# Optimization experiments

Hardware: AMD Instinct MI355X
Metric: run time of the kernel (lower is better)

Reference implementation:

```python
import jax, jax.numpy as jnp
import numpy as np

NEG_BIG = -9e15
ALPHA = 0.2  # LeakyReLU negative slope


def setup_inputs() -> dict:
    key = jax.random.key(0)
    k1, k2, k3, k4 = jax.random.split(key, 4)
    B, N, Fin, Fout = 4, 2048, 128, 128
    h = jax.random.normal(k1, (B, N, Fin), dtype=jnp.float32)
    adj = jax.random.randint(k2, (N, N), 0, 2, dtype=jnp.int32)
    W = jax.random.normal(k3, (Fin, Fout), dtype=jnp.float32) * 0.1
    a = jax.random.normal(k4, (2 * Fout, 1), dtype=jnp.float32) * 0.1
    return {"h": h, "adj": adj, "W": W, "a": a}


def reference(h, adj, W, a):
    # Wh: [B, N, Fout]
    Wh = jnp.einsum('bnf,fo->bno', h, W)
    Fout = W.shape[1]
    a1 = a[:Fout, 0]   # attends to source i
    a2 = a[Fout:, 0]   # attends to target j
    # Decomposed form of leakyrelu(cat([Wh_i, Wh_j]) @ a):
    # e_ij = leakyrelu(a1.Wh_i + a2.Wh_j)  -> [B, N, N]
    f1 = Wh @ a1  # [B, N]
    f2 = Wh @ a2  # [B, N]
    e = jax.nn.leaky_relu(f1[:, :, None] + f2[:, None, :], negative_slope=ALPHA)
    attention = jnp.where(adj[None, :, :] > 0, e, jnp.float32(NEG_BIG))
    attention = jax.nn.softmax(attention, axis=2)
    # dropout is identity in eval mode
    h_prime = jnp.einsum('bij,bjo->bio', attention, Wh)
    return h_prime
```

## Files before the change

kernel.cpp:

```cpp
#include <hip/hip_runtime.h>

#define BB 4
#define NN 2048
#define FF 128
#define NP 2176
#define ALPHA 0.2f
#define SHIFT_C 16.0f

typedef short bf16x8 __attribute__((ext_vector_type(8)));
typedef float f32x4 __attribute__((ext_vector_type(4)));
typedef unsigned u32;

__device__ inline short f2bf(float f) {
    union { float f; unsigned u; } v; v.f = f;
    unsigned r = (v.u + 0x7FFFu + ((v.u >> 16) & 1u)) >> 16;
    return (short)r;
}
__device__ inline float bf2f(short s) {
    union { float f; unsigned u; } v;
    v.u = ((unsigned)(unsigned short)s) << 16;
    return v.f;
}

__global__ __launch_bounds__(256) void k_wh(const float* __restrict__ h,
                                            const float* __restrict__ W,
                                            const float* __restrict__ a,
                                            const int* __restrict__ adj,
                                            short* __restrict__ WhHiT,
                                            short* __restrict__ WhLoT,
                                            float* __restrict__ f1,
                                            float* __restrict__ f2,
                                            u32* __restrict__ adjp) {
    __shared__ float Wa[2 * FF];
    __shared__ float hs[16 * 132];
    int tid = threadIdx.x;
    int r0 = blockIdx.x * 16;

    {
        int fin = tid & 127;
        const float* av = (tid < 128) ? a : (a + FF);
        const float* wr = W + (size_t)fin * FF;
        float s = 0.f;
        for (int o = 0; o < FF; o += 4) {
            float4 wv = *(const float4*)(wr + o);
            float4 avv = *(const float4*)(av + o);
            s += wv.x * avv.x + wv.y * avv.y + wv.z * avv.z + wv.w * avv.w;
        }
        Wa[(tid < 128 ? 0 : FF) + fin] = s;
    }
    {
        const float4* src = (const float4*)(h + (size_t)r0 * FF);
        float4* dst = (float4*)hs;
        dst[tid] = src[tid];
        dst[256 + tid] = src[256 + tid];
    }
    {
        int g = blockIdx.x * 256 + tid;
        int row = g >> 6, wd = g & 63;
        const int4* ar = (const int4*)(adj + (size_t)row * NN + wd * 32);
        u32 word = 0;
#pragma unroll
        for (int q = 0; q < 8; ++q) {
            int4 v = ar[q];
            word |= (u32)(v.x > 0) << (q * 4);
            word |= (u32)(v.y > 0) << (q * 4 + 1);
            word |= (u32)(v.z > 0) << (q * 4 + 2);
            word |= (u32)(v.w > 0) << (q * 4 + 3);
        }
        adjp[row * 64 + wd] = word;
    }
    __syncthreads();

    {
        int w = tid >> 6, lane = tid & 63;
        float wa1_0 = Wa[lane], wa1_1 = Wa[lane + 64];
        float wa2_0 = Wa[FF + lane], wa2_1 = Wa[FF + lane + 64];
        for (int rr = 0; rr < 4; ++rr) {
            int rloc = w * 4 + rr;
            int row = r0 + rloc;
            float x0 = hs[rloc * FF + lane], x1 = hs[rloc * FF + lane + 64];
            float s1 = x0 * wa1_0 + x1 * wa1_1;
            float s2 = x0 * wa2_0 + x1 * wa2_1;
#pragma unroll
            for (int m = 32; m >= 1; m >>= 1) {
                s1 += __shfl_xor(s1, m, 64);
                s2 += __shfl_xor(s2, m, 64);
            }
            if (lane == 0) { f1[row] = s1; f2[row] = s2; }
        }
    }

    int f4 = (tid & 31) * 4;
    int rg = tid >> 5;
    float acc[2][4];
#pragma unroll
    for (int rr = 0; rr < 2; ++rr)
#pragma unroll
        for (int cc = 0; cc < 4; ++cc) acc[rr][cc] = 0.f;

    for (int k0 = 0; k0 < FF; k0 += 4) {
        float4 wv[4];
#pragma unroll
        for (int kk = 0; kk < 4; ++kk)
            wv[kk] = *(const float4*)(W + (size_t)(k0 + kk) * FF + f4);
        float4 hv[2];
#pragma unroll
        for (int rr = 0; rr < 2; ++rr)
            hv[rr] = *(const float4*)(hs + (rg * 2 + rr) * FF + k0);
#pragma unroll
        for (int rr = 0; rr < 2; ++rr) {
            float hk[4] = {hv[rr].x, hv[rr].y, hv[rr].z, hv[rr].w};
#pragma unroll
            for (int kk = 0; kk < 4; ++kk) {
                acc[rr][0] += hk[kk] * wv[kk].x;
                acc[rr][1] += hk[kk] * wv[kk].y;
                acc[rr][2] += hk[kk] * wv[kk].z;
                acc[rr][3] += hk[kk] * wv[kk].w;
            }
        }
    }

    __syncthreads();
    {
#pragma unroll
        for (int rr = 0; rr < 2; ++rr)
            *(float4*)(hs + (rg * 2 + rr) * 132 + f4) =
                make_float4(acc[rr][0], acc[rr][1], acc[rr][2], acc[rr][3]);
    }
    __syncthreads();
    {
        int fo = tid >> 1, jh = tid & 1;
        bf16x8 hv_, lv_;
#pragma unroll
        for (int jj = 0; jj < 8; ++jj) {
            float v = hs[(jh * 8 + jj) * 132 + fo];
            short hh = f2bf(v);
            hv_[jj] = hh;
            lv_[jj] = f2bf(v - bf2f(hh));
        }
        int b = r0 >> 11;
        int j0 = (r0 & (NN - 1)) + jh * 8;
        size_t off = (size_t)(b * FF + fo) * NP + j0;
        *(bf16x8*)(WhHiT + off) = hv_;
        *(bf16x8*)(WhLoT + off) = lv_;
    }
}

#define EV(f2v, f1v, wv, bi) ({ float _t = (f1v) + (f2v); float _x = fmaxf(_t, ALPHA * _t); \
    __expf(_x - SHIFT_C) * (float)(((wv) >> (bi)) & 1u); })

__global__ __launch_bounds__(512, 4) void k_attn(const short* __restrict__ WhHiT,
                                                 const short* __restrict__ WhLoT,
                                                 const u32* __restrict__ adjp,
                                                 const float* __restrict__ f1,
                                                 const float* __restrict__ f2,
                                                 float* __restrict__ out) {
    __shared__ __align__(16) char lds[66688];
    float* row_ps = (float*)(lds + 65536);
    float* row_inv = (float*)(lds + 66560);

    int tid = threadIdx.x;
    int w = tid >> 6, lane = tid & 63;
    int blk = blockIdx.x;
    int b = blk >> 7;
    int tile = (blk >> 1) & 63;
    int half = blk & 1;
    int i0 = tile * 32;

    int r_c = lane & 15, kg = lane >> 4;

    const float* f2b = f2 + b * NN;
    float f10 = f1[b * NN + i0 + r_c];
    float f11 = f1[b * NN + i0 + 16 + r_c];
    const u32* ap0 = adjp + (size_t)(i0 + r_c) * 64;
    const u32* ap1 = adjp + (size_t)(i0 + 16 + r_c) * 64;

    const ptrdiff_t dLo = (ptrdiff_t)BB * FF * NP;
    int s0 = w * 8;
    const short* pB0 = WhHiT + (size_t)(b * FF + half * 64 + 0 * 16 + r_c) * NP + s0 * 32 + kg * 8;
    const short* pB1 = WhHiT + (size_t)(b * FF + half * 64 + 1 * 16 + r_c) * NP + s0 * 32 + kg * 8;
    const short* pB2 = WhHiT + (size_t)(b * FF + half * 64 + 2 * 16 + r_c) * NP + s0 * 32 + kg * 8;
    const short* pB3 = WhHiT + (size_t)(b * FF + half * 64 + 3 * 16 + r_c) * NP + s0 * 32 + kg * 8;

    f32x4 acc0_0 = {0,0,0,0}, acc0_1 = {0,0,0,0};
    f32x4 acc1_0 = {0,0,0,0}, acc1_1 = {0,0,0,0};
    f32x4 acc2_0 = {0,0,0,0}, acc2_1 = {0,0,0,0};
    f32x4 acc3_0 = {0,0,0,0}, acc3_1 = {0,0,0,0};
    float sp0 = 0.f, sp1 = 0.f;

    float4 q0 = *(const float4*)(f2b + s0 * 32 + kg * 8);
    float4 q1 = *(const float4*)(f2b + s0 * 32 + kg * 8 + 4);
    u32 w0 = ap0[s0], w1 = ap1[s0];

#pragma unroll
    for (int s8 = 0; s8 < 8; ++s8) {
        bf16x8 bh0 = *(const bf16x8*)(pB0); bf16x8 bl0 = *(const bf16x8*)(pB0 + dLo);
        bf16x8 bh1 = *(const bf16x8*)(pB1); bf16x8 bl1 = *(const bf16x8*)(pB1 + dLo);
        bf16x8 bh2 = *(const bf16x8*)(pB2); bf16x8 bl2 = *(const bf16x8*)(pB2 + dLo);
        bf16x8 bh3 = *(const bf16x8*)(pB3); bf16x8 bl3 = *(const bf16x8*)(pB3 + dLo);
        int sn = (s0 + s8 + 1) & 63;
        float4 nq0 = *(const float4*)(f2b + sn * 32 + kg * 8);
        float4 nq1 = *(const float4*)(f2b + sn * 32 + kg * 8 + 4);
        u32 nw0 = ap0[sn], nw1 = ap1[sn];

        union { u32 u[4]; bf16x8 v; } A0, A1;
        int bb = kg * 8;
        {
            float pa, pb;
            pa = EV(q0.x, f10, w0, bb + 0); pb = EV(q0.y, f10, w0, bb + 1);
            sp0 += pa + pb;
            asm("v_cvt_pk_bf16_f32 %0, %1, %2" : "=v"(A0.u[0]) : "v"(pa), "v"(pb));
            pa = EV(q0.z, f10, w0, bb + 2); pb = EV(q0.w, f10, w0, bb + 3);
            sp0 += pa + pb;
            asm("v_cvt_pk_bf16_f32 %0, %1, %2" : "=v"(A0.u[1]) : "v"(pa), "v"(pb));
            pa = EV(q1.x, f10, w0, bb + 4); pb = EV(q1.y, f10, w0, bb + 5);
            sp0 += pa + pb;
            asm("v_cvt_pk_bf16_f32 %0, %1, %2" : "=v"(A0.u[2]) : "v"(pa), "v"(pb));
            pa = EV(q1.z, f10, w0, bb + 6); pb = EV(q1.w, f10, w0, bb + 7);
            sp0 += pa + pb;
            asm("v_cvt_pk_bf16_f32 %0, %1, %2" : "=v"(A0.u[3]) : "v"(pa), "v"(pb));

            pa = EV(q0.x, f11, w1, bb + 0); pb = EV(q0.y, f11, w1, bb + 1);
            sp1 += pa + pb;
            asm("v_cvt_pk_bf16_f32 %0, %1, %2" : "=v"(A1.u[0]) : "v"(pa), "v"(pb));
            pa = EV(q0.z, f11, w1, bb + 2); pb = EV(q0.w, f11, w1, bb + 3);
            sp1 += pa + pb;
            asm("v_cvt_pk_bf16_f32 %0, %1, %2" : "=v"(A1.u[1]) : "v"(pa), "v"(pb));
            pa = EV(q1.x, f11, w1, bb + 4); pb = EV(q1.y, f11, w1, bb + 5);
            sp1 += pa + pb;
            asm("v_cvt_pk_bf16_f32 %0, %1, %2" : "=v"(A1.u[2]) : "v"(pa), "v"(pb));
            pa = EV(q1.z, f11, w1, bb + 6); pb = EV(q1.w, f11, w1, bb + 7);
            sp1 += pa + pb;
            asm("v_cvt_pk_bf16_f32 %0, %1, %2" : "=v"(A1.u[3]) : "v"(pa), "v"(pb));
        }

        acc0_0 = __builtin_amdgcn_mfma_f32_16x16x32_bf16(A0.v, bh0, acc0_0, 0, 0, 0);
        acc0_0 = __builtin_amdgcn_mfma_f32_16x16x32_bf16(A0.v, bl0, acc0_0, 0, 0, 0);
        acc0_1 = __builtin_amdgcn_mfma_f32_16x16x32_bf16(A1.v, bh0, acc0_1, 0, 0, 0);
        acc0_1 = __builtin_amdgcn_mfma_f32_16x16x32_bf16(A1.v, bl0, acc0_1, 0, 0, 0);
        acc1_0 = __builtin_amdgcn_mfma_f32_16x16x32_bf16(A0.v, bh1, acc1_0, 0, 0, 0);
        acc1_0 = __builtin_amdgcn_mfma_f32_16x16x32_bf16(A0.v, bl1, acc1_0, 0, 0, 0);
        acc1_1 = __builtin_amdgcn_mfma_f32_16x16x32_bf16(A1.v, bh1, acc1_1, 0, 0, 0);
        acc1_1 = __builtin_amdgcn_mfma_f32_16x16x32_bf16(A1.v, bl1, acc1_1, 0, 0, 0);
        acc2_0 = __builtin_amdgcn_mfma_f32_16x16x32_bf16(A0.v, bh2, acc2_0, 0, 0, 0);
        acc2_0 = __builtin_amdgcn_mfma_f32_16x16x32_bf16(A0.v, bl2, acc2_0, 0, 0, 0);
        acc2_1 = __builtin_amdgcn_mfma_f32_16x16x32_bf16(A1.v, bh2, acc2_1, 0, 0, 0);
        acc2_1 = __builtin_amdgcn_mfma_f32_16x16x32_bf16(A1.v, bl2, acc2_1, 0, 0, 0);
        acc3_0 = __builtin_amdgcn_mfma_f32_16x16x32_bf16(A0.v, bh3, acc3_0, 0, 0, 0);
        acc3_0 = __builtin_amdgcn_mfma_f32_16x16x32_bf16(A0.v, bl3, acc3_0, 0, 0, 0);
        acc3_1 = __builtin_amdgcn_mfma_f32_16x16x32_bf16(A1.v, bh3, acc3_1, 0, 0, 0);
        acc3_1 = __builtin_amdgcn_mfma_f32_16x16x32_bf16(A1.v, bl3, acc3_1, 0, 0, 0);

        pB0 += 32; pB1 += 32; pB2 += 32; pB3 += 32;
        q0 = nq0; q1 = nq1; w0 = nw0; w1 = nw1;
    }

    sp0 += __shfl_xor(sp0, 16, 64); sp0 += __shfl_xor(sp0, 32, 64);
    sp1 += __shfl_xor(sp1, 16, 64); sp1 += __shfl_xor(sp1, 32, 64);
    if (lane < 16) {
        row_ps[w * 32 + lane] = sp0;
        row_ps[w * 32 + 16 + lane] = sp1;
    }
    {
        char* img = lds + w * 8192;
#define STACC(NI, MI, A) { int ch = (((NI)*16 + r_c) * 8 + (MI)*4 + kg) ^ (r_c & 7); \
                           *(f32x4*)(img + ch * 16) = (A); }
        STACC(0, 0, acc0_0) STACC(0, 1, acc0_1)
        STACC(1, 0, acc1_0) STACC(1, 1, acc1_1)
        STACC(2, 0, acc2_0) STACC(2, 1, acc2_1)
        STACC(3, 0, acc3_0) STACC(3, 1, acc3_1)
#undef STACC
    }
    __syncthreads();
    if (tid < 32) {
        float t = 0.f;
#pragma unroll
        for (int ww = 0; ww < 8; ++ww) t += row_ps[ww * 32 + tid];
        row_inv[tid] = 1.0f / t;
    }
    __syncthreads();

    {
        int colg = w * 8 + (lane >> 3);
        int rq = lane & 7;
        int ch = (colg * 8 + rq) ^ (colg & 7);
        f32x4 v = {0, 0, 0, 0};
#pragma unroll
        for (int im = 0; im < 8; ++im)
            v += *(const f32x4*)(lds + im * 8192 + ch * 16);
        f32x4 rinv = *(const f32x4*)((char*)row_inv + rq * 16);
        float* ob = out + ((size_t)b * NN + i0 + rq * 4) * FF + half * 64 + colg;
#pragma unroll
        for (int q = 0; q < 4; ++q)
            ob[(size_t)q * FF] = v[q] * rinv[q];
    }
}

extern "C" void kernel_launch(void* const* d_in, const int* in_sizes, int n_in,
                              void* d_out, int out_size, void* d_ws, size_t ws_size,
                              hipStream_t stream) {
    const float* h   = (const float*)d_in[0];
    const int*   adj = (const int*)d_in[1];
    const float* W   = (const float*)d_in[2];
    const float* a   = (const float*)d_in[3];
    float* out = (float*)d_out;

    short* WhHiT = (short*)d_ws;
    short* WhLoT = WhHiT + (size_t)BB * FF * NP;
    float* f1 = (float*)(WhLoT + (size_t)BB * FF * NP);
    float* f2 = f1 + (size_t)BB * NN;
    u32* adjp = (u32*)(f2 + (size_t)BB * NN);

    k_wh<<<(BB * NN) / 16, 256, 0, stream>>>(h, W, a, adj, WhHiT, WhLoT, f1, f2, adjp);
    k_attn<<<512, 512, 0, stream>>>(WhHiT, WhLoT, adjp, f1, f2, out);
}
```

Measured before the change: 129.3 us.

## Retile attention blocks to 64 rows by 32 output columns

Each block now covers 64 query rows and a quarter of the output features (32 columns) instead of 32 rows and half the features. Each wave builds four attention A-fragments and loads two Wh B-fragment pairs instead of two A-fragments and four B pairs. This cuts global loads of the transposed Wh per block and increases exp/softmax work per block. In exchange the exponentials for each row are recomputed across four column-quarter blocks instead of two, roughly doubling the total VALU exp work. The LDS reduction layout and row-sum buffers are resized to match.

After: 124.4 us (median of 2 runs). -3.8%, faster.

```diff
diff --git a/kernel.cpp b/kernel.cpp
--- a/kernel.cpp
+++ b/kernel.cpp
@@ -149,147 +149,138 @@
 #define EV(f2v, f1v, wv, bi) ({ float _t = (f1v) + (f2v); float _x = fmaxf(_t, ALPHA * _t); \
     __expf(_x - SHIFT_C) * (float)(((wv) >> (bi)) & 1u); })
 
+#define BUILD_A(Adst, F1V, WV, SP) { \
+    float pa, pb; \
+    pa = EV(q0.x, F1V, WV, bb + 0); pb = EV(q0.y, F1V, WV, bb + 1); \
+    SP += pa + pb; \
+    asm("v_cvt_pk_bf16_f32 %0, %1, %2" : "=v"(Adst.u[0]) : "v"(pa), "v"(pb)); \
+    pa = EV(q0.z, F1V, WV, bb + 2); pb = EV(q0.w, F1V, WV, bb + 3); \
+    SP += pa + pb; \
+    asm("v_cvt_pk_bf16_f32 %0, %1, %2" : "=v"(Adst.u[1]) : "v"(pa), "v"(pb)); \
+    pa = EV(q1.x, F1V, WV, bb + 4); pb = EV(q1.y, F1V, WV, bb + 5); \
+    SP += pa + pb; \
+    asm("v_cvt_pk_bf16_f32 %0, %1, %2" : "=v"(Adst.u[2]) : "v"(pa), "v"(pb)); \
+    pa = EV(q1.z, F1V, WV, bb + 6); pb = EV(q1.w, F1V, WV, bb + 7); \
+    SP += pa + pb; \
+    asm("v_cvt_pk_bf16_f32 %0, %1, %2" : "=v"(Adst.u[3]) : "v"(pa), "v"(pb)); }
+
 __global__ __launch_bounds__(512, 4) void k_attn(const short* __restrict__ WhHiT,
                                                  const short* __restrict__ WhLoT,
                                                  const u32* __restrict__ adjp,
                                                  const float* __restrict__ f1,
                                                  const float* __restrict__ f2,
                                                  float* __restrict__ out) {
-    __shared__ __align__(16) char lds[66688];
+    __shared__ __align__(16) char lds[67840];
     float* row_ps = (float*)(lds + 65536);
-    float* row_inv = (float*)(lds + 66560);
+    float* row_inv = (float*)(lds + 67584);
 
     int tid = threadIdx.x;
     int w = tid >> 6, lane = tid & 63;
     int blk = blockIdx.x;
     int b = blk >> 7;
-    int tile = (blk >> 1) & 63;
-    int half = blk & 1;
-    int i0 = tile * 32;
+    int tile = (blk >> 2) & 31;
+    int qt = blk & 3;
+    int i0 = tile * 64;
 
     int r_c = lane & 15, kg = lane >> 4;
 
     const float* f2b = f2 + b * NN;
     float f10 = f1[b * NN + i0 + r_c];
     float f11 = f1[b * NN + i0 + 16 + r_c];
+    float f12 = f1[b * NN + i0 + 32 + r_c];
+    float f13 = f1[b * NN + i0 + 48 + r_c];
     const u32* ap0 = adjp + (size_t)(i0 + r_c) * 64;
     const u32* ap1 = adjp + (size_t)(i0 + 16 + r_c) * 64;
+    const u32* ap2 = adjp + (size_t)(i0 + 32 + r_c) * 64;
+    const u32* ap3 = adjp + (size_t)(i0 + 48 + r_c) * 64;
 
     const ptrdiff_t dLo = (ptrdiff_t)BB * FF * NP;
     int s0 = w * 8;
-    const short* pB0 = WhHiT + (size_t)(b * FF + half * 64 + 0 * 16 + r_c) * NP + s0 * 32 + kg * 8;
-    const short* pB1 = WhHiT + (size_t)(b * FF + half * 64 + 1 * 16 + r_c) * NP + s0 * 32 + kg * 8;
-    const short* pB2 = WhHiT + (size_t)(b * FF + half * 64 + 2 * 16 + r_c) * NP + s0 * 32 + kg * 8;
-    const short* pB3 = WhHiT + (size_t)(b * FF + half * 64 + 3 * 16 + r_c) * NP + s0 * 32 + kg * 8;
-
-    f32x4 acc0_0 = {0,0,0,0}, acc0_1 = {0,0,0,0};
-    f32x4 acc1_0 = {0,0,0,0}, acc1_1 = {0,0,0,0};
-    f32x4 acc2_0 = {0,0,0,0}, acc2_1 = {0,0,0,0};
-    f32x4 acc3_0 = {0,0,0,0}, acc3_1 = {0,0,0,0};
-    float sp0 = 0.f, sp1 = 0.f;
+    const short* pB0 = WhHiT + (size_t)(b * FF + qt * 32 + 0 * 16 + r_c) * NP + s0 * 32 + kg * 8;
+    const short* pB1 = WhHiT + (size_t)(b * FF + qt * 32 + 1 * 16 + r_c) * NP + s0 * 32 + kg * 8;
+
+    f32x4 acc0_0 = {0,0,0,0}, acc0_1 = {0,0,0,0}, acc0_2 = {0,0,0,0}, acc0_3 = {0,0,0,0};
+    f32x4 acc1_0 = {0,0,0,0}, acc1_1 = {0,0,0,0}, acc1_2 = {0,0,0,0}, acc1_3 = {0,0,0,0};
+    float sp0 = 0.f, sp1 = 0.f, sp2 = 0.f, sp3 = 0.f;
 
     float4 q0 = *(const float4*)(f2b + s0 * 32 + kg * 8);
     float4 q1 = *(const float4*)(f2b + s0 * 32 + kg * 8 + 4);
-    u32 w0 = ap0[s0], w1 = ap1[s0];
+    u32 w0 = ap0[s0], w1 = ap1[s0], w2 = ap2[s0], w3 = ap3[s0];
 
 #pragma unroll
     for (int s8 = 0; s8 < 8; ++s8) {
         bf16x8 bh0 = *(const bf16x8*)(pB0); bf16x8 bl0 = *(const bf16x8*)(pB0 + dLo);
         bf16x8 bh1 = *(const bf16x8*)(pB1); bf16x8 bl1 = *(const bf16x8*)(pB1 + dLo);
-        bf16x8 bh2 = *(const bf16x8*)(pB2); bf16x8 bl2 = *(const bf16x8*)(pB2 + dLo);
-        bf16x8 bh3 = *(const bf16x8*)(pB3); bf16x8 bl3 = *(const bf16x8*)(pB3 + dLo);
         int sn = (s0 + s8 + 1) & 63;
         float4 nq0 = *(const float4*)(f2b + sn * 32 + kg * 8);
         float4 nq1 = *(const float4*)(f2b + sn * 32 + kg * 8 + 4);
-        u32 nw0 = ap0[sn], nw1 = ap1[sn];
-
-        union { u32 u[4]; bf16x8 v; } A0, A1;
+        u32 nw0 = ap0[sn], nw1 = ap1[sn], nw2 = ap2[sn], nw3 = ap3[sn];
+
+        union { u32 u[4]; bf16x8 v; } A0, A1, A2, A3;
         int bb = kg * 8;
-        {
-            float pa, pb;
-            pa = EV(q0.x, f10, w0, bb + 0); pb = EV(q0.y, f10, w0, bb + 1);
-            sp0 += pa + pb;
-            asm("v_cvt_pk_bf16_f32 %0, %1, %2" : "=v"(A0.u[0]) : "v"(pa), "v"(pb));
-            pa = EV(q0.z, f10, w0, bb + 2); pb = EV(q0.w, f10, w0, bb + 3);
-            sp0 += pa + pb;
-            asm("v_cvt_pk_bf16_f32 %0, %1, %2" : "=v"(A0.u[1]) : "v"(pa), "v"(pb));
-            pa = EV(q1.x, f10, w0, bb + 4); pb = EV(q1.y, f10, w0, bb + 5);
-            sp0 += pa + pb;
-            asm("v_cvt_pk_bf16_f32 %0, %1, %2" : "=v"(A0.u[2]) : "v"(pa), "v"(pb));
-            pa = EV(q1.z, f10, w0, bb + 6); pb = EV(q1.w, f10, w0, bb + 7);
-            sp0 += pa + pb;
-            asm("v_cvt_pk_bf16_f32 %0, %1, %2" : "=v"(A0.u[3]) : "v"(pa), "v"(pb));
-
-            pa = EV(q0.x, f11, w1, bb + 0); pb = EV(q0.y, f11, w1, bb + 1);
-            sp1 += pa + pb;
-            asm("v_cvt_pk_bf16_f32 %0, %1, %2" : "=v"(A1.u[0]) : "v"(pa), "v"(pb));
-            pa = EV(q0.z, f11, w1, bb + 2); pb = EV(q0.w, f11, w1, bb + 3);
-            sp1 += pa + pb;
-            asm("v_cvt_pk_bf16_f32 %0, %1, %2" : "=v"(A1.u[1]) : "v"(pa), "v"(pb));
-            pa = EV(q1.x, f11, w1, bb + 4); pb = EV(q1.y, f11, w1, bb + 5);
-            sp1 += pa + pb;
-            asm("v_cvt_pk_bf16_f32 %0, %1, %2" : "=v"(A1.u[2]) : "v"(pa), "v"(pb));
-            pa = EV(q1.z, f11, w1, bb + 6); pb = EV(q1.w, f11, w1, bb + 7);
-            sp1 += pa + pb;
-            asm("v_cvt_pk_bf16_f32 %0, %1, %2" : "=v"(A1.u[3]) : "v"(pa), "v"(pb));
-        }
+        BUILD_A(A0, f10, w0, sp0)
+        BUILD_A(A1, f11, w1, sp1)
+        BUILD_A(A2, f12, w2, sp2)
+        BUILD_A(A3, f13, w3, sp3)
 
         acc0_0 = __builtin_amdgcn_mfma_f32_16x16x32_bf16(A0.v, bh0, acc0_0, 0, 0, 0);
         acc0_0 = __builtin_amdgcn_mfma_f32_16x16x32_bf16(A0.v, bl0, acc0_0, 0, 0, 0);
         acc0_1 = __builtin_amdgcn_mfma_f32_16x16x32_bf16(A1.v, bh0, acc0_1, 0, 0, 0);
         acc0_1 = __builtin_amdgcn_mfma_f32_16x16x32_bf16(A1.v, bl0, acc0_1, 0, 0, 0);
+        acc0_2 = __builtin_amdgcn_mfma_f32_16x16x32_bf16(A2.v, bh0, acc0_2, 0, 0, 0);
+        acc0_2 = __builtin_amdgcn_mfma_f32_16x16x32_bf16(A2.v, bl0, acc0_2, 0, 0, 0);
+        acc0_3 = __builtin_amdgcn_mfma_f32_16x16x32_bf16(A3.v, bh0, acc0_3, 0, 0, 0);
+        acc0_3 = __builtin_amdgcn_mfma_f32_16x16x32_bf16(A3.v, bl0, acc0_3, 0, 0, 0);
         acc1_0 = __builtin_amdgcn_mfma_f32_16x16x32_bf16(A0.v, bh1, acc1_0, 0, 0, 0);
         acc1_0 = __builtin_amdgcn_mfma_f32_16x16x32_bf16(A0.v, bl1, acc1_0, 0, 0, 0);
         acc1_1 = __builtin_amdgcn_mfma_f32_16x16x32_bf16(A1.v, bh1, acc1_1, 0, 0, 0);
         acc1_1 = __builtin_amdgcn_mfma_f32_16x16x32_bf16(A1.v, bl1, acc1_1, 0, 0, 0);
-        acc2_0 = __builtin_amdgcn_mfma_f32_16x16x32_bf16(A0.v, bh2, acc2_0, 0, 0, 0);
-        acc2_0 = __builtin_amdgcn_mfma_f32_16x16x32_bf16(A0.v, bl2, acc2_0, 0, 0, 0);
-        acc2_1 = __builtin_amdgcn_mfma_f32_16x16x32_bf16(A1.v, bh2, acc2_1, 0, 0, 0);
-        acc2_1 = __builtin_amdgcn_mfma_f32_16x16x32_bf16(A1.v, bl2, acc2_1, 0, 0, 0);
-        acc3_0 = __builtin_amdgcn_mfma_f32_16x16x32_bf16(A0.v, bh3, acc3_0, 0, 0, 0);
-        acc3_0 = __builtin_amdgcn_mfma_f32_16x16x32_bf16(A0.v, bl3, acc3_0, 0, 0, 0);
-        acc3_1 = __builtin_amdgcn_mfma_f32_16x16x32_bf16(A1.v, bh3, acc3_1, 0, 0, 0);
-        acc3_1 = __builtin_amdgcn_mfma_f32_16x16x32_bf16(A1.v, bl3, acc3_1, 0, 0, 0);
-
-        pB0 += 32; pB1 += 32; pB2 += 32; pB3 += 32;
-        q0 = nq0; q1 = nq1; w0 = nw0; w1 = nw1;
+        acc1_2 = __builtin_amdgcn_mfma_f32_16x16x32_bf16(A2.v, bh1, acc1_2, 0, 0, 0);
+        acc1_2 = __builtin_amdgcn_mfma_f32_16x16x32_bf16(A2.v, bl1, acc1_2, 0, 0, 0);
+        acc1_3 = __builtin_amdgcn_mfma_f32_16x16x32_bf16(A3.v, bh1, acc1_3, 0, 0, 0);
+        acc1_3 = __builtin_amdgcn_mfma_f32_16x16x32_bf16(A3.v, bl1, acc1_3, 0, 0, 0);
+
+        pB0 += 32; pB1 += 32;
+        q0 = nq0; q1 = nq1; w0 = nw0; w1 = nw1; w2 = nw2; w3 = nw3;
     }
 
     sp0 += __shfl_xor(sp0, 16, 64); sp0 += __shfl_xor(sp0, 32, 64);
     sp1 += __shfl_xor(sp1, 16, 64); sp1 += __shfl_xor(sp1, 32, 64);
+    sp2 += __shfl_xor(sp2, 16, 64); sp2 += __shfl_xor(sp2, 32, 64);
+    sp3 += __shfl_xor(sp3, 16, 64); sp3 += __shfl_xor(sp3, 32, 64);
     if (lane < 16) {
-        row_ps[w * 32 + lane] = sp0;
-        row_ps[w * 32 + 16 + lane] = sp1;
+        row_ps[w * 64 + lane]      = sp0;
+        row_ps[w * 64 + 16 + lane] = sp1;
+        row_ps[w * 64 + 32 + lane] = sp2;
+        row_ps[w * 64 + 48 + lane] = sp3;
     }
     {
         char* img = lds + w * 8192;
-#define STACC(NI, MI, A) { int ch = (((NI)*16 + r_c) * 8 + (MI)*4 + kg) ^ (r_c & 7); \
+#define STACC(NI, MI, A) { int ch = (((NI)*16 + r_c) * 16 + (MI)*4 + kg) ^ (r_c & 7); \
                            *(f32x4*)(img + ch * 16) = (A); }
-        STACC(0, 0, acc0_0) STACC(0, 1, acc0_1)
-        STACC(1, 0, acc1_0) STACC(1, 1, acc1_1)
-        STACC(2, 0, acc2_0) STACC(2, 1, acc2_1)
-        STACC(3, 0, acc3_0) STACC(3, 1, acc3_1)
+        STACC(0, 0, acc0_0) STACC(0, 1, acc0_1) STACC(0, 2, acc0_2) STACC(0, 3, acc0_3)
+        STACC(1, 0, acc1_0) STACC(1, 1, acc1_1) STACC(1, 2, acc1_2) STACC(1, 3, acc1_3)
 #undef STACC
     }
     __syncthreads();
-    if (tid < 32) {
+    if (tid < 64) {
         float t = 0.f;
 #pragma unroll
-        for (int ww = 0; ww < 8; ++ww) t += row_ps[ww * 32 + tid];
+        for (int ww = 0; ww < 8; ++ww) t += row_ps[ww * 64 + tid];
         row_inv[tid] = 1.0f / t;
     }
     __syncthreads();
 
     {
-        int colg = w * 8 + (lane >> 3);
-        int rq = lane & 7;
-        int ch = (colg * 8 + rq) ^ (colg & 7);
+        int colg = w * 4 + (lane >> 4);
+        int rq = lane & 15;
+        int ch = (colg * 16 + rq) ^ (colg & 7);
         f32x4 v = {0, 0, 0, 0};
 #pragma unroll
         for (int im = 0; im < 8; ++im)
             v += *(const f32x4*)(lds + im * 8192 + ch * 16);
         f32x4 rinv = *(const f32x4*)((char*)row_inv + rq * 16);
-        float* ob = out + ((size_t)b * NN + i0 + rq * 4) * FF + half * 64 + colg;
+        float* ob = out + ((size_t)b * NN + i0 + rq * 4) * FF + qt * 32 + colg;
 #pragma unroll
         for (int q = 0; q < 4; ++q)
             ob[(size_t)q * FF] = v[q] * rinv[q];
```
